# Performance work log

Hardware: AMD Instinct MI355X
Metric: run time of the kernel (lower is better)

Reference implementation:

```python
import jax, jax.numpy as jnp
import numpy as np

NUM_HEADS = 32
NUM_KV_HEADS = 8
HEAD_DIM = 128
ROPE_THETA = 10000.0
NEG_INF = -1e9


def _rope_cos_sin(position_ids, head_dim, dtype):
    # inv_freq: [head_dim/2]
    inv_freq = 1.0 / (ROPE_THETA ** (jnp.arange(0, head_dim, 2, dtype=jnp.float32) / head_dim))
    # freqs: [B, S, head_dim/2]
    freqs = position_ids.astype(jnp.float32)[..., None] * inv_freq[None, None, :]
    emb = jnp.concatenate([freqs, freqs], axis=-1)  # [B, S, head_dim]
    return jnp.cos(emb).astype(dtype), jnp.sin(emb).astype(dtype)


def _rotate_half(x):
    x1, x2 = jnp.split(x, 2, axis=-1)
    return jnp.concatenate([-x2, x1], axis=-1)


def setup_inputs() -> dict:
    key = jax.random.key(0)
    k1, k2, k3, k4, k5 = jax.random.split(key, 5)
    B, S, H = 2, 2048, 4096
    scale = 1.0 / np.sqrt(H)
    return {
        "hidden_states": jax.random.normal(k1, (B, S, H), jnp.float32),
        "position_ids": jnp.broadcast_to(jnp.arange(S, dtype=jnp.int32)[None, :], (B, S)),
        "Wq": jax.random.normal(k2, (H, H), jnp.float32) * scale,
        "Wk": jax.random.normal(k3, (NUM_KV_HEADS * HEAD_DIM, H), jnp.float32) * scale,
        "Wv": jax.random.normal(k4, (NUM_KV_HEADS * HEAD_DIM, H), jnp.float32) * scale,
        "Wo": jax.random.normal(k5, (H, H), jnp.float32) * scale,
    }


def reference(hidden_states, position_ids, Wq, Wk, Wv, Wo):
    B, S, H = hidden_states.shape
    dtype = hidden_states.dtype
    n_rep = NUM_HEADS // NUM_KV_HEADS

    # QKV projections (torch Linear: x @ W.T)
    q = (hidden_states @ Wq.T).reshape(B, S, NUM_HEADS, HEAD_DIM).transpose(0, 2, 1, 3)
    k = (hidden_states @ Wk.T).reshape(B, S, NUM_KV_HEADS, HEAD_DIM).transpose(0, 2, 1, 3)
    v = (hidden_states @ Wv.T).reshape(B, S, NUM_KV_HEADS, HEAD_DIM).transpose(0, 2, 1, 3)

    # RoPE (cos/sin broadcast over heads)
    cos, sin = _rope_cos_sin(position_ids, HEAD_DIM, dtype)
    cos, sin = cos[:, None, :, :], sin[:, None, :, :]  # [B,1,S,D]
    q = q * cos + _rotate_half(q) * sin
    k = k * cos + _rotate_half(k) * sin

    # repeat_kv (GQA): [B, KVH, S, D] -> [B, KVH*n_rep, S, D]
    k = jnp.repeat(k, n_rep, axis=1)
    v = jnp.repeat(v, n_rep, axis=1)

    # scaled dot-product attention with causal mask, softmax in fp32
    scores = jnp.einsum('bhqd,bhkd->bhqk', q, k) / np.sqrt(HEAD_DIM)
    causal = jnp.tril(jnp.ones((S, S), dtype=bool))
    scores = jnp.where(causal[None, None, :, :], scores, NEG_INF)
    probs = jax.nn.softmax(scores.astype(jnp.float32), axis=-1).astype(dtype)

    attn = jnp.einsum('bhqk,bhkd->bhqd', probs, v)
    attn = attn.transpose(0, 2, 1, 3).reshape(B, S, H)
    return attn @ Wo.T
```

## Files before the change

### kernel.cpp

```cpp
#include <hip/hip_runtime.h>

#define S_LEN 2048
#define BATCH 2
#define HID 4096
#define NH 32
#define NKV 8
#define DH 128
#define MROWS (BATCH*S_LEN)
#define QKV_N 6144

typedef unsigned short u16;
typedef unsigned int u32;
typedef __bf16 bf16x8 __attribute__((ext_vector_type(8)));
typedef float f32x4 __attribute__((ext_vector_type(4)));
typedef u16 u16x8 __attribute__((ext_vector_type(8)));

__device__ __forceinline__ u16 f2bf(float f) {
  union { float f; u32 u; } v; v.f = f;
  return (u16)((v.u + 0x8000u) >> 16);
}
__device__ __forceinline__ float bf2f(u16 h) {
  union { u32 u; float f; } v; v.u = ((u32)h) << 16;
  return v.f;
}
__device__ __forceinline__ u32 cvtpk(float a, float b) {
  u32 r;
  asm("v_cvt_pk_bf16_f32 %0, %1, %2" : "=v"(r) : "v"(a), "v"(b));
  return r;
}
__device__ __forceinline__ void async16(const void* g, void* l) {
  __builtin_amdgcn_global_load_lds(
      (const __attribute__((address_space(1))) u32*)g,
      (__attribute__((address_space(3))) u32*)l, 16, 0, 0);
}

__global__ __launch_bounds__(256) void cvt_f32_bf16(const float* __restrict__ in,
                                                    u16* __restrict__ out, int n) {
  int i0 = (blockIdx.x * 256 + threadIdx.x) * 8;
  if (i0 >= n) return;
  float4 a = *(const float4*)(in + i0);
  float4 b = *(const float4*)(in + i0 + 4);
  u16x8 r;
  r[0]=f2bf(a.x); r[1]=f2bf(a.y); r[2]=f2bf(a.z); r[3]=f2bf(a.w);
  r[4]=f2bf(b.x); r[5]=f2bf(b.y); r[6]=f2bf(b.z); r[7]=f2bf(b.w);
  *(u16x8*)(out + i0) = r;
}

template<int OUT_BF16>
__global__ __launch_bounds__(256) void gemm_nt(
    const u16* __restrict__ A, const u16* __restrict__ B, void* __restrict__ Cout,
    int M, int N, int K) {
  __shared__ u16 Al[2][128*32];
  __shared__ u16 Bl[2][128*32];
  int nTN = N >> 7;
  int nwg = gridDim.x;
  int id = ((int)blockIdx.x & 7) * (nwg >> 3) + ((int)blockIdx.x >> 3);
  int tm = id / nTN, tn = id % nTN;
  int m0 = tm << 7, n0 = tn << 7;
  int t = threadIdx.x;
  int w = t >> 6, lane = t & 63, lo = lane & 15, hi = lane >> 4;
  int wr = w >> 1, wc = w & 1;
  int rowA = (w << 4) + (lane >> 2);
  int ccA = lane & 3;

  const f32x4 fz = {0.f, 0.f, 0.f, 0.f};
  f32x4 acc[4][4];
#pragma unroll
  for (int i = 0; i < 4; ++i)
#pragma unroll
    for (int j = 0; j < 4; ++j) acc[i][j] = fz;

  int NK = K >> 5;
  auto stage = [&](int buf, int kt) {
    int k0 = kt << 5;
#pragma unroll
    for (int r = 0; r < 2; ++r) {
      const u16* g = A + (size_t)(m0 + (r << 6) + rowA) * K + k0 + ccA * 8;
      async16(g, (char*)&Al[buf][0] + (r << 12) + (w << 10));
    }
#pragma unroll
    for (int r = 0; r < 2; ++r) {
      const u16* g = B + (size_t)(n0 + (r << 6) + rowA) * K + k0 + ccA * 8;
      async16(g, (char*)&Bl[buf][0] + (r << 12) + (w << 10));
    }
  };

  stage(0, 0);
  int cur = 0;
  for (int kt = 0; kt < NK; ++kt) {
    __syncthreads();
    if (kt + 1 < NK) stage(cur ^ 1, kt + 1);
    bf16x8 af[4], bfv[4];
#pragma unroll
    for (int i = 0; i < 4; ++i)
      af[i] = *(const bf16x8*)(&Al[cur][((wr << 6) + (i << 4) + lo) * 32 + hi * 8]);
#pragma unroll
    for (int j = 0; j < 4; ++j)
      bfv[j] = *(const bf16x8*)(&Bl[cur][((wc << 6) + (j << 4) + lo) * 32 + hi * 8]);
#pragma unroll
    for (int i = 0; i < 4; ++i)
#pragma unroll
      for (int j = 0; j < 4; ++j)
        acc[i][j] = __builtin_amdgcn_mfma_f32_16x16x32_bf16(af[i], bfv[j], acc[i][j], 0, 0, 0);
    cur ^= 1;
  }

#pragma unroll
  for (int i = 0; i < 4; ++i)
#pragma unroll
    for (int j = 0; j < 4; ++j)
#pragma unroll
      for (int r = 0; r < 4; ++r) {
        int row = m0 + (wr << 6) + (i << 4) + (hi << 2) + r;
        int col = n0 + (wc << 6) + (j << 4) + lo;
        if (OUT_BF16) ((u16*)Cout)[(size_t)row * N + col] = f2bf(acc[i][j][r]);
        else          ((float*)Cout)[(size_t)row * N + col] = acc[i][j][r];
      }
}

__global__ __launch_bounds__(256) void rope_kernel(u16* __restrict__ X,
                                                   const int* __restrict__ pos,
                                                   int ncols, int pitch, float scale) {
  int idx = blockIdx.x * 256 + threadIdx.x;
  int groups = ncols >> 3;
  int m = idx / groups;
  int gi = idx - m * groups;
  if (m >= MROWS) return;
  int head = gi >> 4;
  int d0 = (gi & 15) << 2;
  float p = (float)pos[m];
  u16* base = X + (size_t)m * pitch + head * 128;
  u16 xa[4], xb[4], oa[4], ob[4];
  *(uint2*)xa = *(const uint2*)(base + d0);
  *(uint2*)xb = *(const uint2*)(base + d0 + 64);
#pragma unroll
  for (int i = 0; i < 4; ++i) {
    float j = (float)(d0 + i);
    float inv = __expf(j * -0.14391156516030342f);
    float fr = p * inv;
    float s, c;
    sincosf(fr, &s, &c);
    float x1 = bf2f(xa[i]), x2 = bf2f(xb[i]);
    oa[i] = f2bf((x1 * c - x2 * s) * scale);
    ob[i] = f2bf((x2 * c + x1 * s) * scale);
  }
  *(uint2*)(base + d0) = *(uint2*)oa;
  *(uint2*)(base + d0 + 64) = *(uint2*)ob;
}

__global__ __launch_bounds__(256) void transpose_v(const u16* __restrict__ V,
                                                   u16* __restrict__ Vt) {
  int bid = blockIdx.x;
  int s0 = (bid & 31) << 6;
  int bg = bid >> 5;
  int b = bg >> 3, g = bg & 7;
  __shared__ u16 tile[64][128];
  int t = threadIdx.x;
#pragma unroll
  for (int r = 0; r < 4; ++r) {
    int c = (r << 8) + t;
    int row = c >> 4, cc = c & 15;
    *(uint4*)&tile[row][cc * 8] =
        *(const uint4*)(V + (size_t)(b * S_LEN + s0 + row) * QKV_N + g * 128 + cc * 8);
  }
  __syncthreads();
#pragma unroll
  for (int r = 0; r < 4; ++r) {
    int c = (r << 8) + t;
    int d = c >> 3, cs = c & 7;
    u16 tmp[8];
#pragma unroll
    for (int i = 0; i < 8; ++i) tmp[i] = tile[cs * 8 + i][d];
    *(uint4*)(Vt + ((size_t)bg * 128 + d) * S_LEN + s0 + cs * 8) = *(uint4*)tmp;
  }
}

__global__ __launch_bounds__(256) void attn_kernel(
    const u16* __restrict__ Q, const u16* __restrict__ K,
    const u16* __restrict__ Vt, u16* __restrict__ O) {
  int bid = blockIdx.x;
  int qt = 31 - (bid >> 6);
  int bh = bid & 63;
  int b = bh >> 5, h = bh & 31;
  int g = h >> 2;
  __shared__ u16 Kl[64 * 128];
  __shared__ u16 Vl[128 * 64];
  __shared__ u16 Pl[4][16 * 72];
  int t = threadIdx.x, w = t >> 6, lane = t & 63, lo = lane & 15, hi = lane >> 4;

  bf16x8 qf[4];
  {
    const u16* qb = Q + (size_t)(b * S_LEN + (qt << 6) + (w << 4) + lo) * QKV_N + h * 128;
#pragma unroll
    for (int kk = 0; kk < 4; ++kk) qf[kk] = *(const bf16x8*)(qb + kk * 32 + hi * 8);
  }
  const f32x4 fz = {0.f, 0.f, 0.f, 0.f};
  f32x4 acc[8];
#pragma unroll
  for (int f = 0; f < 8; ++f) acc[f] = fz;
  float mrun = -1e30f, lrun = 0.f;

  const u16* Kbase = K + (size_t)(b * S_LEN) * QKV_N + g * 128;
  const u16* Vbase = Vt + (size_t)((b << 3) + g) * 128 * S_LEN;

  int ntiles = qt + 1;
  for (int tile = 0; tile < ntiles; ++tile) {
    int s0 = tile << 6;
#pragma unroll
    for (int r = 0; r < 4; ++r) {
      int c = (r << 8) + (w << 6) + lane;
      int row = c >> 4, cc = c & 15;
      int src = cc ^ (row & 7);
      async16(Kbase + (size_t)(s0 + row) * QKV_N + src * 8,
              (char*)Kl + (r << 12) + (w << 10));
    }
#pragma unroll
    for (int r = 0; r < 4; ++r) {
      int c = (r << 8) + (w << 6) + lane;
      int row = c >> 3, cc = c & 7;
      int src = cc ^ (row & 7);
      async16(Vbase + (size_t)row * S_LEN + s0 + src * 8,
              (char*)Vl + (r << 12) + (w << 10));
    }
    __syncthreads();

    f32x4 sf[4];
#pragma unroll
    for (int j = 0; j < 4; ++j) {
      f32x4 sv = fz;
#pragma unroll
      for (int kk = 0; kk < 4; ++kk) {
        int row = (j << 4) + lo;
        int ch = ((kk << 2) + hi) ^ (row & 7);
        bf16x8 kf = *(const bf16x8*)(Kl + row * 128 + ch * 8);
        sv = __builtin_amdgcn_mfma_f32_16x16x32_bf16(kf, qf[kk], sv, 0, 0, 0);
      }
      sf[j] = sv;
    }
    if (tile == qt) {
      int q_rel = (w << 4) + lo;
#pragma unroll
      for (int j = 0; j < 4; ++j)
#pragma unroll
        for (int r = 0; r < 4; ++r)
          if (((j << 4) + (hi << 2) + r) > q_rel) sf[j][r] = -1e9f;
    }
    float pmax = sf[0][0];
#pragma unroll
    for (int j = 0; j < 4; ++j)
#pragma unroll
      for (int r = 0; r < 4; ++r) pmax = fmaxf(pmax, sf[j][r]);
    pmax = fmaxf(pmax, __shfl_xor(pmax, 16, 64));
    pmax = fmaxf(pmax, __shfl_xor(pmax, 32, 64));
    if (__any(pmax > mrun + 8.f)) {
      float mn = fmaxf(mrun, pmax);
      float fsc = __expf(mrun - mn);
      mrun = mn;
      lrun *= fsc;
#pragma unroll
      for (int f = 0; f < 8; ++f)
#pragma unroll
        for (int r = 0; r < 4; ++r) acc[f][r] *= fsc;
    }
    float psum = 0.f;
#pragma unroll
    for (int j = 0; j < 4; ++j)
#pragma unroll
      for (int r = 0; r < 4; ++r) {
        float p = __expf(sf[j][r] - mrun);
        sf[j][r] = p;
        psum += p;
      }
    psum += __shfl_xor(psum, 16, 64);
    psum += __shfl_xor(psum, 32, 64);
    lrun += psum;

#pragma unroll
    for (int j = 0; j < 4; ++j) {
      uint2 pk;
      pk.x = cvtpk(sf[j][0], sf[j][1]);
      pk.y = cvtpk(sf[j][2], sf[j][3]);
      *(uint2*)&Pl[w][lo * 72 + (j << 4) + (hi << 2)] = pk;
    }
#pragma unroll
    for (int kk = 0; kk < 2; ++kk) {
      bf16x8 pf = *(const bf16x8*)&Pl[w][lo * 72 + (kk << 5) + (hi << 3)];
#pragma unroll
      for (int f = 0; f < 8; ++f) {
        int vrow = (f << 4) + lo;
        int phys = ((kk << 2) + hi) ^ (vrow & 7);
        bf16x8 vf = *(const bf16x8*)(Vl + vrow * 64 + phys * 8);
        acc[f] = __builtin_amdgcn_mfma_f32_16x16x32_bf16(vf, pf, acc[f], 0, 0, 0);
      }
    }
    __syncthreads();
  }

  float rl = 1.0f / lrun;
#pragma unroll
  for (int half = 0; half < 2; ++half) {
#pragma unroll
    for (int f2 = 0; f2 < 4; ++f2) {
      int f = (half << 2) + f2;
      uint2 pk;
      pk.x = cvtpk(acc[f][0] * rl, acc[f][1] * rl);
      pk.y = cvtpk(acc[f][2] * rl, acc[f][3] * rl);
      *(uint2*)&Pl[w][lo * 72 + (f2 << 4) + (hi << 2)] = pk;
    }
#pragma unroll
    for (int it = 0; it < 2; ++it) {
      int rowq = (lane >> 3) + (it << 3);
      int c8 = lane & 7;
      uint4 val = *(const uint4*)&Pl[w][rowq * 72 + c8 * 8];
      *(uint4*)(O + (size_t)(b * S_LEN + (qt << 6) + (w << 4) + rowq) * 4096 +
                h * 128 + (half << 6) + c8 * 8) = val;
    }
  }
}

extern "C" void kernel_launch(void* const* d_in, const int* in_sizes, int n_in,
                              void* d_out, int out_size, void* d_ws, size_t ws_size,
                              hipStream_t stream) {
  const float* hidden = (const float*)d_in[0];
  const int* pos = (const int*)d_in[1];
  const float* Wq = (const float*)d_in[2];
  const float* Wk = (const float*)d_in[3];
  const float* Wv = (const float*)d_in[4];
  const float* Wo = (const float*)d_in[5];
  float* out = (float*)d_out;

  u16* hb   = (u16*)d_ws;
  u16* wqb  = hb   + 16777216;
  u16* wkb  = wqb  + 16777216;
  u16* wvb  = wkb  + 4194304;
  u16* wob  = wvb  + 4194304;
  u16* QKVb = wob  + 16777216;
  u16* Vtb  = QKVb + 25165824;
  u16* Ob   = Vtb  + 4194304;

  cvt_f32_bf16<<<8192, 256, 0, stream>>>(hidden, hb, 16777216);
  cvt_f32_bf16<<<8192, 256, 0, stream>>>(Wq, wqb, 16777216);
  cvt_f32_bf16<<<2048, 256, 0, stream>>>(Wk, wkb, 4194304);
  cvt_f32_bf16<<<2048, 256, 0, stream>>>(Wv, wvb, 4194304);
  cvt_f32_bf16<<<8192, 256, 0, stream>>>(Wo, wob, 16777216);

  gemm_nt<1><<<1536, 256, 0, stream>>>(hb, wqb, QKVb, 4096, QKV_N, 4096);

  rope_kernel<<<8192, 256, 0, stream>>>(QKVb, pos, 4096, QKV_N, 0.08838834764831845f);
  rope_kernel<<<2048, 256, 0, stream>>>(QKVb + 4096, pos, 1024, QKV_N, 1.0f);

  transpose_v<<<512, 256, 0, stream>>>(QKVb + 5120, Vtb);

  attn_kernel<<<2048, 256, 0, stream>>>(QKVb, QKVb + 4096, Vtb, Ob);

  gemm_nt<0><<<1024, 256, 0, stream>>>(Ob, wob, out, 4096, 4096, 4096);
}
```

Measured before the change: 613.9 us.

## Replace 128x128 GEMM with 256x256 tiled, swizzled, interleaved-pipeline GEMM

```diff
diff --git a/kernel.cpp b/kernel.cpp
--- a/kernel.cpp
+++ b/kernel.cpp
@@ -32,6 +32,9 @@
   __builtin_amdgcn_global_load_lds(
       (const __attribute__((address_space(1))) u32*)g,
       (__attribute__((address_space(3))) u32*)l, 16, 0, 0);
+}
+__device__ __forceinline__ f32x4 mfma16(bf16x8 a, bf16x8 b, f32x4 c) {
+  return __builtin_amdgcn_mfma_f32_16x16x32_bf16(a, b, c, 0, 0, 0);
 }
 
 __global__ __launch_bounds__(256) void cvt_f32_bf16(const float* __restrict__ in,
@@ -47,74 +50,161 @@
 }
 
 template<int OUT_BF16>
-__global__ __launch_bounds__(256) void gemm_nt(
+__global__ __launch_bounds__(512, 2) void gemm256(
     const u16* __restrict__ A, const u16* __restrict__ B, void* __restrict__ Cout,
     int M, int N, int K) {
-  __shared__ u16 Al[2][128*32];
-  __shared__ u16 Bl[2][128*32];
-  int nTN = N >> 7;
+  __shared__ u16 As[2][2][64 * 128];
+  __shared__ u16 Bs[2][2][64 * 128];
+  const int NKT = K >> 6;
+  int nTN = N >> 8;
   int nwg = gridDim.x;
   int id = ((int)blockIdx.x & 7) * (nwg >> 3) + ((int)blockIdx.x >> 3);
   int tm = id / nTN, tn = id % nTN;
-  int m0 = tm << 7, n0 = tn << 7;
+  int m0 = tm << 8, n0 = tn << 8;
   int t = threadIdx.x;
   int w = t >> 6, lane = t & 63, lo = lane & 15, hi = lane >> 4;
-  int wr = w >> 1, wc = w & 1;
-  int rowA = (w << 4) + (lane >> 2);
-  int ccA = lane & 3;
+  int wm = w >> 2, wn = w & 3;
+  int rbb = (wn & 1) << 6;
+
+  int srow = (w << 3) + (lane >> 3);
+  int scol = (lane & 7) << 3;
+
+  auto stageA = [&](int kt, int buf, int h) {
+#pragma unroll
+    for (int c2 = 0; c2 < 2; ++c2) {
+      int row = (c2 << 6) + srow;
+      int col = scol ^ ((row & 4) << 2);
+      async16(A + (size_t)(m0 + (h << 7) + row) * K + (kt << 6) + col,
+              (char*)&As[buf][h][0] + (c2 << 13) + (w << 10));
+    }
+  };
+  auto stageB = [&](int kt, int buf, int h) {
+#pragma unroll
+    for (int c2 = 0; c2 < 2; ++c2) {
+      int row = (c2 << 6) + srow;
+      int col = scol ^ ((row & 4) << 2);
+      async16(B + (size_t)(n0 + (h << 7) + row) * K + (kt << 6) + col,
+              (char*)&Bs[buf][h][0] + (c2 << 13) + (w << 10));
+    }
+  };
 
   const f32x4 fz = {0.f, 0.f, 0.f, 0.f};
-  f32x4 acc[4][4];
-#pragma unroll
-  for (int i = 0; i < 4; ++i)
+  f32x4 acc[8][4];
+#pragma unroll
+  for (int i = 0; i < 8; ++i)
 #pragma unroll
     for (int j = 0; j < 4; ++j) acc[i][j] = fz;
-
-  int NK = K >> 5;
-  auto stage = [&](int buf, int kt) {
-    int k0 = kt << 5;
-#pragma unroll
-    for (int r = 0; r < 2; ++r) {
-      const u16* g = A + (size_t)(m0 + (r << 6) + rowA) * K + k0 + ccA * 8;
-      async16(g, (char*)&Al[buf][0] + (r << 12) + (w << 10));
-    }
-#pragma unroll
-    for (int r = 0; r < 2; ++r) {
-      const u16* g = B + (size_t)(n0 + (r << 6) + rowA) * K + k0 + ccA * 8;
-      async16(g, (char*)&Bl[buf][0] + (r << 12) + (w << 10));
-    }
-  };
-
-  stage(0, 0);
-  int cur = 0;
-  for (int kt = 0; kt < NK; ++kt) {
-    __syncthreads();
-    if (kt + 1 < NK) stage(cur ^ 1, kt + 1);
-    bf16x8 af[4], bfv[4];
-#pragma unroll
-    for (int i = 0; i < 4; ++i)
-      af[i] = *(const bf16x8*)(&Al[cur][((wr << 6) + (i << 4) + lo) * 32 + hi * 8]);
-#pragma unroll
-    for (int j = 0; j < 4; ++j)
-      bfv[j] = *(const bf16x8*)(&Bl[cur][((wc << 6) + (j << 4) + lo) * 32 + hi * 8]);
-#pragma unroll
-    for (int i = 0; i < 4; ++i)
-#pragma unroll
-      for (int j = 0; j < 4; ++j)
-        acc[i][j] = __builtin_amdgcn_mfma_f32_16x16x32_bf16(af[i], bfv[j], acc[i][j], 0, 0, 0);
-    cur ^= 1;
-  }
-
-#pragma unroll
-  for (int i = 0; i < 4; ++i)
-#pragma unroll
-    for (int j = 0; j < 4; ++j)
+  bf16x8 af[4][2], bfr[4][2];
+
+  stageB(0, 0, 0); stageB(0, 0, 1);
+  stageA(0, 0, 0); stageA(0, 0, 1);
+  stageB(1, 1, 0); stageB(1, 1, 1);
+  asm volatile("s_waitcnt vmcnt(4)" ::: "memory");
+  __builtin_amdgcn_s_barrier();
+
+  for (int kt = 0; kt < NKT; ++kt) {
+    int c = kt & 1;
+    const u16* Ab = &As[c][wm][0];
+    const u16* Bb = &Bs[c][wn >> 1][0];
+    int kn1 = (kt + 1 == NKT) ? 0 : kt + 1;
+    int kn2 = (kt + 2 >= NKT) ? kt + 2 - NKT : kt + 2;
+
+#pragma unroll
+    for (int mf = 0; mf < 4; ++mf)
+#pragma unroll
+      for (int ks = 0; ks < 2; ++ks) {
+        int ra = (mf << 4) + lo;
+        af[mf][ks] = *(const bf16x8*)(Ab + (ra << 6) +
+                      (((ks << 5) + (hi << 3)) ^ ((ra & 4) << 2)));
+      }
+#pragma unroll
+    for (int nf = 0; nf < 2; ++nf)
+#pragma unroll
+      for (int ks = 0; ks < 2; ++ks) {
+        int rb = rbb + (nf << 4) + lo;
+        bfr[nf][ks] = *(const bf16x8*)(Bb + (rb << 6) +
+                      (((ks << 5) + (hi << 3)) ^ ((rb & 4) << 2)));
+      }
+    stageA(kn1, c ^ 1, 0);
+    __builtin_amdgcn_s_barrier();
+    __builtin_amdgcn_s_setprio(1);
+#pragma unroll
+    for (int mf = 0; mf < 4; ++mf)
+#pragma unroll
+      for (int nf = 0; nf < 2; ++nf)
+#pragma unroll
+        for (int ks = 0; ks < 2; ++ks)
+          acc[mf][nf] = mfma16(af[mf][ks], bfr[nf][ks], acc[mf][nf]);
+    __builtin_amdgcn_s_setprio(0);
+    __builtin_amdgcn_s_barrier();
+
+#pragma unroll
+    for (int nf = 0; nf < 2; ++nf)
+#pragma unroll
+      for (int ks = 0; ks < 2; ++ks) {
+        int rb = rbb + ((nf + 2) << 4) + lo;
+        bfr[nf + 2][ks] = *(const bf16x8*)(Bb + (rb << 6) +
+                      (((ks << 5) + (hi << 3)) ^ ((rb & 4) << 2)));
+      }
+    stageA(kn1, c ^ 1, 1);
+    __builtin_amdgcn_s_barrier();
+    __builtin_amdgcn_s_setprio(1);
+#pragma unroll
+    for (int mf = 0; mf < 4; ++mf)
+#pragma unroll
+      for (int nf = 0; nf < 2; ++nf)
+#pragma unroll
+        for (int ks = 0; ks < 2; ++ks)
+          acc[mf][nf + 2] = mfma16(af[mf][ks], bfr[nf + 2][ks], acc[mf][nf + 2]);
+    __builtin_amdgcn_s_setprio(0);
+    __builtin_amdgcn_s_barrier();
+
+#pragma unroll
+    for (int mf = 0; mf < 4; ++mf)
+#pragma unroll
+      for (int ks = 0; ks < 2; ++ks) {
+        int ra = 64 + (mf << 4) + lo;
+        af[mf][ks] = *(const bf16x8*)(Ab + (ra << 6) +
+                      (((ks << 5) + (hi << 3)) ^ ((ra & 4) << 2)));
+      }
+    stageB(kn2, c, 0);
+    __builtin_amdgcn_s_barrier();
+    __builtin_amdgcn_s_setprio(1);
+#pragma unroll
+    for (int mf = 0; mf < 4; ++mf)
+#pragma unroll
+      for (int nf = 0; nf < 2; ++nf)
+#pragma unroll
+        for (int ks = 0; ks < 2; ++ks)
+          acc[mf + 4][nf + 2] = mfma16(af[mf][ks], bfr[nf + 2][ks], acc[mf + 4][nf + 2]);
+    __builtin_amdgcn_s_setprio(0);
+    __builtin_amdgcn_s_barrier();
+
+    stageB(kn2, c, 1);
+    __builtin_amdgcn_s_barrier();
+    __builtin_amdgcn_s_setprio(1);
+#pragma unroll
+    for (int mf = 0; mf < 4; ++mf)
+#pragma unroll
+      for (int nf = 0; nf < 2; ++nf)
+#pragma unroll
+        for (int ks = 0; ks < 2; ++ks)
+          acc[mf + 4][nf] = mfma16(af[mf][ks], bfr[nf][ks], acc[mf + 4][nf]);
+    __builtin_amdgcn_s_setprio(0);
+    asm volatile("s_waitcnt vmcnt(4)" ::: "memory");
+    __builtin_amdgcn_s_barrier();
+  }
+
+#pragma unroll
+  for (int mf = 0; mf < 8; ++mf)
+#pragma unroll
+    for (int nf = 0; nf < 4; ++nf)
 #pragma unroll
       for (int r = 0; r < 4; ++r) {
-        int row = m0 + (wr << 6) + (i << 4) + (hi << 2) + r;
-        int col = n0 + (wc << 6) + (j << 4) + lo;
-        if (OUT_BF16) ((u16*)Cout)[(size_t)row * N + col] = f2bf(acc[i][j][r]);
-        else          ((float*)Cout)[(size_t)row * N + col] = acc[i][j][r];
+        int row = m0 + (wm << 7) + (mf << 4) + (hi << 2) + r;
+        int col = n0 + (wn << 6) + (nf << 4) + lo;
+        if (OUT_BF16) ((u16*)Cout)[(size_t)row * N + col] = f2bf(acc[mf][nf][r]);
+        else          ((float*)Cout)[(size_t)row * N + col] = acc[mf][nf][r];
       }
 }
 
@@ -344,7 +434,7 @@
   cvt_f32_bf16<<<2048, 256, 0, stream>>>(Wv, wvb, 4194304);
   cvt_f32_bf16<<<8192, 256, 0, stream>>>(Wo, wob, 16777216);
 
-  gemm_nt<1><<<1536, 256, 0, stream>>>(hb, wqb, QKVb, 4096, QKV_N, 4096);
+  gemm256<1><<<384, 512, 0, stream>>>(hb, wqb, QKVb, 4096, QKV_N, 4096);
 
   rope_kernel<<<8192, 256, 0, stream>>>(QKVb, pos, 4096, QKV_N, 0.08838834764831845f);
   rope_kernel<<<2048, 256, 0, stream>>>(QKVb + 4096, pos, 1024, QKV_N, 1.0f);
@@ -353,5 +443,5 @@
 
   attn_kernel<<<2048, 256, 0, stream>>>(QKVb, QKVb + 4096, Vtb, Ob);
 
-  gemm_nt<0><<<1024, 256, 0, stream>>>(Ob, wob, out, 4096, 4096, 4096);
-}
+  gemm256<0><<<256, 512, 0, stream>>>(Ob, wob, out, 4096, 4096, 4096);
+}
```

Result: no change. 625.1 us (+1.8%).
